# Performance work log

Hardware: AMD Instinct MI355X
Metric: run time of the kernel (lower is better)

## Reference

```python
import jax, jax.numpy as jnp
import numpy as np

B, T, F, M = 32, 256, 512, 4   # batch, pred_len (=d_model=state_size), feature_dim (=mamba seq), time-mark feats
N = F - M                      # number of variates in x_enc
T2 = 2 * T
EPS = 1e-5


def setup_inputs() -> dict:
    key = jax.random.key(0)
    it = iter(jax.random.split(key, 32))
    def nrm(*s):
        return jax.random.normal(next(it), s, jnp.float32) * 0.02
    inp = {
        "x_enc": jax.random.normal(next(it), (B, T, N), jnp.float32),
        "x_mark_enc": jax.random.normal(next(it), (B, T, M), jnp.float32),
        "x_dec": jnp.zeros((1, 1, 1), jnp.float32),
        "x_mark_dec": jnp.zeros((1, 1, 1), jnp.float32),
        # 3 structurally identical MambaBlocks -> stack params on leading dim 3
        "norm_w": jnp.ones((3, T), jnp.float32),
        "inp_W": nrm(3, T, T2), "inp_b": jnp.zeros((3, T2), jnp.float32),
        "conv_W": nrm(3, F, F, 3), "conv_b": jnp.zeros((3, F), jnp.float32),
        "convlin_W": nrm(3, T2, T2), "convlin_b": jnp.zeros((3, T2), jnp.float32),
        "fc1_W": nrm(3, T2, T2), "fc1_b": jnp.zeros((3, T2), jnp.float32),
        "fc2_W": nrm(3, T2, T), "fc2_b": jnp.zeros((3, T), jnp.float32),
        "fc3_W": nrm(3, T2, T), "fc3_b": jnp.zeros((3, T), jnp.float32),
        "D_W": nrm(3, T, T2), "D_b": jnp.zeros((3, T2), jnp.float32),
        "out_W": nrm(3, T2, T), "out_b": jnp.ones((3, T), jnp.float32),  # out_proj.bias init to 1.0
        "proj_W": nrm(T, T), "proj_b": jnp.zeros((T,), jnp.float32),
    }
    return inp


def _rmsnorm(x, w):
    return x * jax.lax.rsqrt(jnp.mean(x * x, -1, keepdims=True) + EPS) * w


def _conv1d(x, W, b):
    # x: [B, C, L], W: [C_out, C_in, 3], padding=1
    y = jax.lax.conv_general_dilated(x, W, (1,), [(1, 1)], dimension_numbers=("NCH", "OIH", "NCH"))
    return y + b[None, :, None]


def _s6(x, fc1W, fc1b, fc2W, fc2b, fc3W, fc3b):
    # h is zero-initialized each call, so dA=exp(delta*A) multiplies zeros and
    # y = einsum('bln,bldn->bld', C, x[...,None]*dB) = delta * x * <C,B>_n
    Bmat = x @ fc2W + fc2b                         # [B, L, n]
    Cmat = x @ fc3W + fc3b                         # [B, L, n]
    delta = jax.nn.softplus(x @ fc1W + fc1b)       # [B, L, d]
    cb = jnp.einsum("bln,bln->bl", Cmat, Bmat)   # contraction over state dim
    return delta * x * cb[:, :, None]


def _block(x, i, p):
    xn = _rmsnorm(x, p["norm_w"][i])
    xp = xn @ p["inp_W"][i] + p["inp_b"][i]                      # [B, F, 2T]
    xc = jax.nn.silu(_conv1d(xp, p["conv_W"][i], p["conv_b"][i]))
    xco = xc @ p["convlin_W"][i] + p["convlin_b"][i]
    xssm = _s6(xco, p["fc1_W"][i], p["fc1_b"][i], p["fc2_W"][i], p["fc2_b"][i], p["fc3_W"][i], p["fc3_b"][i])
    xres = jax.nn.silu(xn @ p["D_W"][i] + p["D_b"][i])
    return (jax.nn.silu(xssm) * xres) @ p["out_W"][i] + p["out_b"][i]


def _forward(x_enc, x_mark_enc, p):
    means = jax.lax.stop_gradient(jnp.mean(x_enc, 1, keepdims=True))  # detached in torch
    xe = x_enc - means
    stdev = jnp.sqrt(jnp.var(xe, axis=1, keepdims=True) + 1e-5)       # NOT detached in torch
    xe = xe / stdev
    x = jnp.concatenate([xe, x_mark_enc], axis=2).transpose(0, 2, 1)  # [B, F, T]
    for i in range(3):
        x = _block(x, i, p)
    dec = (x @ p["proj_W"] + p["proj_b"]).transpose(0, 2, 1)          # [B, T, F]
    return dec[:, :, :N] * stdev + means                              # pred_len == T


def reference(x_enc, x_mark_enc, x_dec, x_mark_dec, norm_w, inp_W, inp_b, conv_W, conv_b, convlin_W, convlin_b, fc1_W, fc1_b, fc2_W, fc2_b, fc3_W, fc3_b, D_W, D_b, out_W, out_b, proj_W, proj_b):
    p = dict(norm_w=norm_w, inp_W=inp_W, inp_b=inp_b, conv_W=conv_W, conv_b=conv_b, convlin_W=convlin_W, convlin_b=convlin_b, fc1_W=fc1_W, fc1_b=fc1_b, fc2_W=fc2_W, fc2_b=fc2_b, fc3_W=fc3_W, fc3_b=fc3_b, D_W=D_W, D_b=D_b, out_W=out_W, out_b=out_b, proj_W=proj_W, proj_b=proj_b)
    return _forward(x_enc, x_mark_enc, p)
```

## Files before the change

### kernel.cpp

```cpp
#include <hip/hip_runtime.h>
#include <hip/hip_bf16.h>
#include <math.h>

typedef __hip_bfloat16 bf16;
typedef short short8 __attribute__((ext_vector_type(8)));
typedef short short4v __attribute__((ext_vector_type(4)));
typedef float floatx4 __attribute__((ext_vector_type(4)));

constexpr int CB_ = 32;
constexpr int CT = 256;
constexpr int CF = 512;
constexpr int CN = 508;
constexpr int CM = 4;
constexpr int CT2 = 512;
constexpr int MROWS = CB_ * CF;
constexpr int PADL = 528;

__device__ __forceinline__ float b2f(bf16 v) { return __bfloat162float(v); }
__device__ __forceinline__ bf16 f2b(float v) { return __float2bfloat16(v); }
__device__ __forceinline__ float s2f(short s) {
    unsigned u = ((unsigned)(unsigned short)s) << 16;
    return __builtin_bit_cast(float, u);
}
__device__ __forceinline__ short f2s(float v) {
    bf16 t = __float2bfloat16(v);
    return __builtin_bit_cast(short, t);
}
__device__ __forceinline__ float silu_f(float x) { return x / (1.0f + __expf(-x)); }
__device__ __forceinline__ float softplus_f(float x) {
    return fmaxf(x, 0.0f) + __logf(1.0f + __expf(-fabsf(x)));
}

__device__ __forceinline__ void gl_lds16(const bf16* g, short* l) {
    __builtin_amdgcn_global_load_lds(
        (const __attribute__((address_space(1))) unsigned int*)(g),
        (__attribute__((address_space(3))) unsigned int*)(l), 16, 0, 0);
}

constexpr int CONVN = 3 * 3 * 512 * 512;
constexpr int MTILES = 3520;
struct P8 { const float* s[8]; bf16* d[8]; };
__global__ __launch_bounds__(256) void prepack_all_kernel(P8 p, const float* __restrict__ nw,
                                                          const float* __restrict__ convW,
                                                          bf16* __restrict__ convD,
                                                          bf16* __restrict__ xpT,
                                                          float* __restrict__ CBv) {
    int bid = blockIdx.x;
    if (bid >= MTILES) {
        int idx = (bid - MTILES) * 256 + threadIdx.x;
        if (idx < CONVN) {
            int ci = idx & 511;
            int co = (idx >> 9) & 511;
            int it = idx >> 18;
            int tap = it % 3, ib = it / 3;
            convD[idx] = f2b(convW[(((size_t)(ib * 512 + co)) * 512 + ci) * 3 + tap]);
        } else if (idx < CONVN + 32768) {
            int j = idx - CONVN;
            int ci = j & 511;
            int w = (j >> 9) & 1;
            int b = j >> 10;
            xpT[((size_t)b * PADL + (w ? 513 : 0)) * 512 + ci] = f2b(0.0f);
        } else if (idx < CONVN + 32768 + MROWS) {
            CBv[idx - CONVN - 32768] = 0.0f;
        }
        return;
    }
    const int Ks[8]   = {256, 256, 512, 512, 512, 512, 512, 256};
    const int Ns[8]   = {512, 512, 512, 256, 256, 512, 256, 256};
    const int zs[8]   = {3, 3, 3, 3, 3, 3, 3, 1};
    const int dstr[8] = {262144, 262144, 524288, 524288, 524288, 262144, 131072, 65536};
    const int rml[8]  = {1, 1, 1, 2, 2, 1, 1, 1};
    const int rad[8]  = {0, 0, 0, 0, 1, 0, 0, 0};
    int m = 0, acc = 0;
    for (m = 0; m < 8; m++) {
        int c = (Ns[m] >> 5) * (Ks[m] >> 5) * zs[m];
        if (bid < acc + c) break;
        acc += c;
    }
    int lid = bid - acc;
    int K = Ks[m], N = Ns[m];
    int tx = N >> 5, ty = K >> 5;
    int z = lid / (tx * ty), rem = lid % (tx * ty);
    int k0 = (rem / tx) * 32, n0 = (rem % tx) * 32;
    const float* s = p.s[m] + (size_t)z * K * N;
    bf16* d = p.d[m] + (size_t)z * dstr[m];
    int mul = rml[m], add = rad[m];
    bool fold = (m <= 1);
    __shared__ float Ts[32][33];
    for (int e = threadIdx.x; e < 1024; e += 256) {
        int r = e >> 5, c = e & 31;
        float v = s[(size_t)(k0 + r) * N + n0 + c];
        if (fold) v *= nw[z * 256 + k0 + r];
        Ts[r][c] = v;
    }
    __syncthreads();
    for (int e = threadIdx.x; e < 1024; e += 256) {
        int r = e >> 5, c = e & 31;
        d[(size_t)((n0 + r) * mul + add) * K + k0 + c] = f2b(Ts[c][r]);
    }
}

__global__ __launch_bounds__(256) void buildx_kernel(
    const float* __restrict__ xe, const float* __restrict__ xm,
    float* __restrict__ means, float* __restrict__ stdev,
    bf16* __restrict__ X0, float* __restrict__ SCL) {
    __shared__ float L[256][65];
    __shared__ float red_s[4][64], red_q[4][64];
    __shared__ float stat_m[64], stat_i[64];
    int blk = blockIdx.x;
    int b = blk >> 3, f0 = (blk & 7) * 64;
    int tid = threadIdx.x;
    int j = tid & 63, tq = tid >> 6;
    int f = f0 + j;
    float ps = 0.f, pq = 0.f;
    const float* xep = xe + (size_t)b * CT * CN + f;
    const float* xmp = xm + (size_t)b * CT * CM + (f - CN);
    #pragma unroll 4
    for (int tt = 0; tt < 64; tt++) {
        int t = tq * 64 + tt;
        float v = (f < CN) ? xep[(size_t)t * CN] : xmp[(size_t)t * CM];
        L[t][j] = v;
        ps += v;
        pq += v * v;
    }
    red_s[tq][j] = ps;
    red_q[tq][j] = pq;
    __syncthreads();
    if (tid < 64) {
        int ff = f0 + tid;
        float s = red_s[0][tid] + red_s[1][tid] + red_s[2][tid] + red_s[3][tid];
        float q = red_q[0][tid] + red_q[1][tid] + red_q[2][tid] + red_q[3][tid];
        float mean, isd, msq;
        if (ff < CN) {
            mean = s * (1.0f / 256.0f);
            float var = fmaxf(q * (1.0f / 256.0f) - mean * mean, 0.0f);
            float sd = sqrtf(var + 1e-5f);
            isd = 1.0f / sd;
            means[b * CN + ff] = mean;
            stdev[b * CN + ff] = sd;
            msq = var / (var + 1e-5f);
        } else {
            mean = 0.0f;
            isd = 1.0f;
            msq = q * (1.0f / 256.0f);
        }
        stat_m[tid] = mean;
        stat_i[tid] = isd;
        SCL[b * 512 + ff] = rsqrtf(msq + 1e-5f);
    }
    __syncthreads();
    bf16* outp = X0 + ((size_t)(b * 512 + f0)) * 256;
    int t = tid;
    #pragma unroll 4
    for (int fp = 0; fp < 64; fp++) {
        float val = (L[t][fp] - stat_m[fp]) * stat_i[fp];
        outp[(size_t)fp * 256 + t] = f2b(val);
    }
}

template <int MODE>
__global__ __launch_bounds__(256) void mgemm_kernel(const bf16* __restrict__ A,
                                                    const bf16* __restrict__ Wt,
                                                    const float* __restrict__ b1,
                                                    const float* __restrict__ b2,
                                                    const float* __restrict__ SCL,
                                                    bf16* __restrict__ o1,
                                                    bf16* __restrict__ o2,
                                                    int K, int Ncols) {
    __shared__ __align__(16) short As[128 * 32];
    __shared__ __align__(16) short Bs[128 * 32];
    const int tid = threadIdx.x;
    const int lane = tid & 63;
    const int wave = tid >> 6;
    const int m0 = blockIdx.x * 128, n0 = blockIdx.y * 128;

    const int srow0 = wave * 32;
    const int lrow = lane >> 2;
    const int lcol = (lane & 3) * 8;

    const bf16* aP0 = A + (size_t)(m0 + srow0 + lrow) * K + lcol;
    const bf16* aP1 = A + (size_t)(m0 + srow0 + 16 + lrow) * K + lcol;
    const bf16* bP0 = Wt + (size_t)(n0 + srow0 + lrow) * K + lcol;
    const bf16* bP1 = Wt + (size_t)(n0 + srow0 + 16 + lrow) * K + lcol;
    short* aL0 = &As[srow0 * 32];
    short* aL1 = &As[(srow0 + 16) * 32];
    short* bL0 = &Bs[srow0 * 32];
    short* bL1 = &Bs[(srow0 + 16) * 32];

    const int wm = (wave & 1) * 64, wn = (wave >> 1) * 64;
    const int fr = lane & 15, quad = lane >> 4;

    floatx4 acc[4][4];
    #pragma unroll
    for (int i = 0; i < 4; i++)
        #pragma unroll
        for (int j = 0; j < 4; j++) acc[i][j] = (floatx4){0.f, 0.f, 0.f, 0.f};

    for (int k0 = 0; k0 < K; k0 += 32) {
        gl_lds16(aP0 + k0, aL0);
        gl_lds16(aP1 + k0, aL1);
        gl_lds16(bP0 + k0, bL0);
        gl_lds16(bP1 + k0, bL1);
        __syncthreads();
        short8 af[4], bfv[4];
        #pragma unroll
        for (int i = 0; i < 4; i++) af[i] = *(const short8*)&As[(wm + i * 16 + fr) * 32 + quad * 8];
        #pragma unroll
        for (int j = 0; j < 4; j++) bfv[j] = *(const short8*)&Bs[(wn + j * 16 + fr) * 32 + quad * 8];
        #pragma unroll
        for (int i = 0; i < 4; i++)
            #pragma unroll
            for (int j = 0; j < 4; j++)
                acc[i][j] = __builtin_amdgcn_mfma_f32_16x16x32_bf16(af[i], bfv[j], acc[i][j], 0, 0, 0);
        __syncthreads();
    }

    if (MODE == 0) {
        #pragma unroll
        for (int j = 0; j < 4; j++) {
            int n = n0 + wn + j * 16 + fr;
            float bv = b1[n];
            #pragma unroll
            for (int i = 0; i < 4; i++) {
                int mb = m0 + wm + i * 16 + quad * 4;
                #pragma unroll
                for (int r = 0; r < 4; r++)
                    o1[(size_t)(mb + r) * Ncols + n] = f2b(acc[i][j][r] + bv);
            }
        }
    } else {
        if (n0 + wn < 512) {
            int b = (m0 + wm) >> 9;
            #pragma unroll
            for (int i = 0; i < 4; i++) {
                int mb = m0 + wm + i * 16 + quad * 4;
                float sclr[4];
                #pragma unroll
                for (int r = 0; r < 4; r++) sclr[r] = SCL[mb + r];
                #pragma unroll
                for (int j = 0; j < 4; j++) {
                    int n = n0 + wn + j * 16 + fr;
                    float bv = b1[n];
                    bf16* dst = o1 + ((size_t)b * PADL + n + 1) * 512;
                    int ci = mb & 511;
                    short4v pk;
                    #pragma unroll
                    for (int r = 0; r < 4; r++) pk[r] = f2s(acc[i][j][r] * sclr[r] + bv);
                    *(short4v*)(dst + ci) = pk;
                }
            }
        } else {
            #pragma unroll
            for (int i = 0; i < 4; i++) {
                int mb = m0 + wm + i * 16 + quad * 4;
                float sclr[4];
                #pragma unroll
                for (int r = 0; r < 4; r++) sclr[r] = SCL[mb + r];
                #pragma unroll
                for (int j = 0; j < 4; j++) {
                    int n = n0 + wn + j * 16 + fr;
                    float bv = b2[n - 512];
                    #pragma unroll
                    for (int r = 0; r < 4; r++)
                        o2[(size_t)(mb + r) * 512 + (n - 512)] =
                            f2b(silu_f(acc[i][j][r] * sclr[r] + bv));
                }
            }
        }
    }
}

__global__ __launch_bounds__(256) void cbgemm_kernel(const bf16* __restrict__ A,
                                                     const bf16* __restrict__ Wt,
                                                     const float* __restrict__ b2,
                                                     const float* __restrict__ b3,
                                                     float* __restrict__ CBv) {
    __shared__ __align__(16) short As[128 * 32];
    __shared__ __align__(16) short Bs[128 * 32];
    const int tid = threadIdx.x;
    const int lane = tid & 63;
    const int wave = tid >> 6;
    const int m0 = blockIdx.x * 128, n0 = blockIdx.y * 128;

    const int srow0 = wave * 32;
    const int lrow = lane >> 2;
    const int lcol = (lane & 3) * 8;
    const bf16* aP0 = A + (size_t)(m0 + srow0 + lrow) * 512 + lcol;
    const bf16* aP1 = A + (size_t)(m0 + srow0 + 16 + lrow) * 512 + lcol;
    const bf16* bP0 = Wt + (size_t)(n0 + srow0 + lrow) * 512 + lcol;
    const bf16* bP1 = Wt + (size_t)(n0 + srow0 + 16 + lrow) * 512 + lcol;
    short* aL0 = &As[srow0 * 32];
    short* aL1 = &As[(srow0 + 16) * 32];
    short* bL0 = &Bs[srow0 * 32];
    short* bL1 = &Bs[(srow0 + 16) * 32];

    const int wm = (wave & 1) * 64, wn = (wave >> 1) * 64;
    const int fr = lane & 15, quad = lane >> 4;

    floatx4 acc[4][4];
    #pragma unroll
    for (int i = 0; i < 4; i++)
        #pragma unroll
        for (int j = 0; j < 4; j++) acc[i][j] = (floatx4){0.f, 0.f, 0.f, 0.f};

    for (int k0 = 0; k0 < 512; k0 += 32) {
        gl_lds16(aP0 + k0, aL0);
        gl_lds16(aP1 + k0, aL1);
        gl_lds16(bP0 + k0, bL0);
        gl_lds16(bP1 + k0, bL1);
        __syncthreads();
        short8 af[4], bfv[4];
        #pragma unroll
        for (int i = 0; i < 4; i++) af[i] = *(const short8*)&As[(wm + i * 16 + fr) * 32 + quad * 8];
        #pragma unroll
        for (int j = 0; j < 4; j++) bfv[j] = *(const short8*)&Bs[(wn + j * 16 + fr) * 32 + quad * 8];
        #pragma unroll
        for (int i = 0; i < 4; i++)
            #pragma unroll
            for (int j = 0; j < 4; j++)
                acc[i][j] = __builtin_amdgcn_mfma_f32_16x16x32_bf16(af[i], bfv[j], acc[i][j], 0, 0, 0);
        __syncthreads();
    }
    int nnb = n0 + wn;
    float bv[4];
    #pragma unroll
    for (int j = 0; j < 4; j++) {
        int nn = nnb + j * 16 + fr;
        int c = nn >> 1;
        bv[j] = (fr & 1) ? b3[c] : b2[c];
    }
    #pragma unroll
    for (int i = 0; i < 4; i++) {
        #pragma unroll
        for (int r = 0; r < 4; r++) {
            float s = 0.f;
            #pragma unroll
            for (int j = 0; j < 4; j++) {
                float v = acc[i][j][r] + bv[j];
                s += v * __shfl_xor(v, 1);
            }
            s += __shfl_xor(s, 2);
            s += __shfl_xor(s, 4);
            s += __shfl_xor(s, 8);
            if (fr == 0)
                atomicAdd(&CBv[m0 + wm + i * 16 + quad * 4 + r], s * 0.5f);
        }
    }
}

__global__ __launch_bounds__(256) void fc1gate_kernel(const bf16* __restrict__ A,
                                                      const bf16* __restrict__ Wt,
                                                      const float* __restrict__ b1,
                                                      const float* __restrict__ CBv,
                                                      const bf16* __restrict__ Xres,
                                                      bf16* __restrict__ G) {
    __shared__ __align__(16) short As[128 * 32];
    __shared__ __align__(16) short Bs[128 * 32];
    const int tid = threadIdx.x;
    const int lane = tid & 63;
    const int wave = tid >> 6;
    const int m0 = blockIdx.x * 128, n0 = blockIdx.y * 128;

    const int srow0 = wave * 32;
    const int lrow = lane >> 2;
    const int lcol = (lane & 3) * 8;
    const bf16* aP0 = A + (size_t)(m0 + srow0 + lrow) * 512 + lcol;
    const bf16* aP1 = A + (size_t)(m0 + srow0 + 16 + lrow) * 512 + lcol;
    const bf16* bP0 = Wt + (size_t)(n0 + srow0 + lrow) * 512 + lcol;
    const bf16* bP1 = Wt + (size_t)(n0 + srow0 + 16 + lrow) * 512 + lcol;
    short* aL0 = &As[srow0 * 32];
    short* aL1 = &As[(srow0 + 16) * 32];
    short* bL0 = &Bs[srow0 * 32];
    short* bL1 = &Bs[(srow0 + 16) * 32];

    const int wm = (wave & 1) * 64, wn = (wave >> 1) * 64;
    const int fr = lane & 15, quad = lane >> 4;

    floatx4 acc[4][4];
    #pragma unroll
    for (int i = 0; i < 4; i++)
        #pragma unroll
        for (int j = 0; j < 4; j++) acc[i][j] = (floatx4){0.f, 0.f, 0.f, 0.f};

    for (int k0 = 0; k0 < 512; k0 += 32) {
        gl_lds16(aP0 + k0, aL0);
        gl_lds16(aP1 + k0, aL1);
        gl_lds16(bP0 + k0, bL0);
        gl_lds16(bP1 + k0, bL1);
        __syncthreads();
        short8 af[4], bfv[4];
        #pragma unroll
        for (int i = 0; i < 4; i++) af[i] = *(const short8*)&As[(wm + i * 16 + fr) * 32 + quad * 8];
        #pragma unroll
        for (int j = 0; j < 4; j++) bfv[j] = *(const short8*)&Bs[(wn + j * 16 + fr) * 32 + quad * 8];
        #pragma unroll
        for (int i = 0; i < 4; i++)
            #pragma unroll
            for (int j = 0; j < 4; j++)
                acc[i][j] = __builtin_amdgcn_mfma_f32_16x16x32_bf16(af[i], bfv[j], acc[i][j], 0, 0, 0);
        __syncthreads();
    }
    #pragma unroll
    for (int i = 0; i < 4; i++) {
        int mb = m0 + wm + i * 16 + quad * 4;
        float cbr[4];
        #pragma unroll
        for (int r = 0; r < 4; r++) cbr[r] = CBv[mb + r];
        #pragma unroll
        for (int j = 0; j < 4; j++) {
            int n = n0 + wn + j * 16 + fr;
            float bv = b1[n];
            #pragma unroll
            for (int r = 0; r < 4; r++) {
                size_t off = (size_t)(mb + r) * 512 + n;
                float delta = softplus_f(acc[i][j][r] + bv);
                float xssm = delta * b2f(A[off]) * cbr[r];
                G[off] = f2b(silu_f(xssm) * b2f(Xres[off]));
            }
        }
    }
}

__global__ __launch_bounds__(256) void conv_mfma_kernel(const bf16* __restrict__ Wc,
                                                        const bf16* __restrict__ xpT,
                                                        const float* __restrict__ bias,
                                                        bf16* __restrict__ Out,
                                                        float* __restrict__ CBvZ) {
    __shared__ __align__(16) short As[3 * 128 * 32];
    __shared__ __align__(16) short Bs[144 * 32];
    const int tid = threadIdx.x;
    const int lane = tid & 63;
    const int wave = tid >> 6;
    int bx = blockIdx.x;
    if (bx < 128 && tid < 128) CBvZ[bx * 128 + tid] = 0.0f;
    int xcd = bx & 7, g = bx >> 3;
    int mt = g & 3;
    int id = xcd * 16 + (g >> 2);
    int nt = id & 3, b = id >> 2;
    const int m0 = mt * 128, n0 = nt * 128;
    const bf16* xb = xpT + (size_t)b * PADL * 512;

    const int lrow = lane >> 2;
    const int lcol = (lane & 3) * 8;
    const int wm = (wave & 1) * 64, wn = (wave >> 1) * 64;
    const int fr = lane & 15, quad = lane >> 4;

    floatx4 acc[4][4];
    #pragma unroll
    for (int i = 0; i < 4; i++)
        #pragma unroll
        for (int j = 0; j < 4; j++) acc[i][j] = (floatx4){0.f, 0.f, 0.f, 0.f};

    for (int k0 = 0; k0 < 512; k0 += 32) {
        for (int ga = wave; ga < 24; ga += 4) {
            int tap = ga >> 3, rg = ga & 7;
            gl_lds16(Wc + (size_t)tap * 262144 + (size_t)(m0 + rg * 16 + lrow) * 512 + k0 + lcol,
                     &As[ga * 512]);
        }
        for (int gb = wave; gb < 9; gb += 4) {
            gl_lds16(xb + (size_t)(n0 + gb * 16 + lrow) * 512 + k0 + lcol, &Bs[gb * 512]);
        }
        __syncthreads();
        #pragma unroll
        for (int tap = 0; tap < 3; tap++) {
            short8 af[4], bfv[4];
            #pragma unroll
            for (int i = 0; i < 4; i++)
                af[i] = *(const short8*)&As[tap * 4096 + (wm + i * 16 + fr) * 32 + quad * 8];
            #pragma unroll
            for (int j = 0; j < 4; j++)
                bfv[j] = *(const short8*)&Bs[(wn + j * 16 + fr + tap) * 32 + quad * 8];
            #pragma unroll
            for (int i = 0; i < 4; i++)
                #pragma unroll
                for (int j = 0; j < 4; j++)
                    acc[i][j] = __builtin_amdgcn_mfma_f32_16x16x32_bf16(af[i], bfv[j], acc[i][j], 0, 0, 0);
        }
        __syncthreads();
    }
    bf16* ob = Out + (size_t)b * CF * CT2;
    #pragma unroll
    for (int i = 0; i < 4; i++) {
        int mb = m0 + wm + i * 16 + quad * 4;
        #pragma unroll
        for (int r = 0; r < 4; r++) {
            float bv = bias[mb + r];
            #pragma unroll
            for (int j = 0; j < 4; j++) {
                int n = n0 + wn + j * 16 + fr;
                ob[(size_t)(mb + r) * CT2 + n] = f2b(silu_f(acc[i][j][r] + bv));
            }
        }
    }
}

__global__ __launch_bounds__(256) void gemm_scl_kernel(const bf16* __restrict__ A,
                                                       const bf16* __restrict__ Wt,
                                                       const float* __restrict__ bias,
                                                       bf16* __restrict__ Xo,
                                                       float* __restrict__ SCL) {
    __shared__ __align__(16) short As[64 * 32];
    __shared__ __align__(16) short Bs[256 * 32];
    __shared__ float red[4][64];
    const int tid = threadIdx.x;
    const int lane = tid & 63;
    const int wave = tid >> 6;
    const int m0 = blockIdx.x * 64;

    const int lrow = lane >> 2;
    const int lcol = (lane & 3) * 8;
    const bf16* aP = A + (size_t)(m0 + wave * 16 + lrow) * 512 + lcol;
    short* aL = &As[wave * 16 * 32];
    const bf16* bP[4];
    short* bL[4];
    #pragma unroll
    for (int g = 0; g < 4; g++) {
        int r0 = (wave * 4 + g) * 16;
        bP[g] = Wt + (size_t)(r0 + lrow) * 512 + lcol;
        bL[g] = &Bs[r0 * 32];
    }
    const int wn = wave * 64;
    const int fr = lane & 15, quad = lane >> 4;

    floatx4 acc[4][4];
    #pragma unroll
    for (int i = 0; i < 4; i++)
        #pragma unroll
        for (int j = 0; j < 4; j++) acc[i][j] = (floatx4){0.f, 0.f, 0.f, 0.f};

    for (int k0 = 0; k0 < 512; k0 += 32) {
        gl_lds16(aP + k0, aL);
        #pragma unroll
        for (int g = 0; g < 4; g++) gl_lds16(bP[g] + k0, bL[g]);
        __syncthreads();
        short8 af[4], bfv[4];
        #pragma unroll
        for (int i = 0; i < 4; i++) af[i] = *(const short8*)&As[(i * 16 + fr) * 32 + quad * 8];
        #pragma unroll
        for (int j = 0; j < 4; j++) bfv[j] = *(const short8*)&Bs[(wn + j * 16 + fr) * 32 + quad * 8];
        #pragma unroll
        for (int i = 0; i < 4; i++)
            #pragma unroll
            for (int j = 0; j < 4; j++)
                acc[i][j] = __builtin_amdgcn_mfma_f32_16x16x32_bf16(af[i], bfv[j], acc[i][j], 0, 0, 0);
        __syncthreads();
    }
    #pragma unroll
    for (int j = 0; j < 4; j++) {
        float bv = bias[wn + j * 16 + fr];
        #pragma unroll
        for (int i = 0; i < 4; i++)
            #pragma unroll
            for (int r = 0; r < 4; r++) acc[i][j][r] += bv;
    }
    #pragma unroll
    for (int i = 0; i < 4; i++) {
        #pragma unroll
        for (int r = 0; r < 4; r++) {
            float s = 0.f;
            #pragma unroll
            for (int j = 0; j < 4; j++) s += acc[i][j][r] * acc[i][j][r];
            #pragma unroll
            for (int o = 8; o > 0; o >>= 1) s += __shfl_xor(s, o);
            if (fr == 0) red[wave][i * 16 + quad * 4 + r] = s;
        }
    }
    __syncthreads();
    if (tid < 64) {
        float tot = red[0][tid] + red[1][tid] + red[2][tid] + red[3][tid];
        SCL[m0 + tid] = rsqrtf(tot * (1.0f / CT) + 1e-5f);
    }
    #pragma unroll
    for (int j = 0; j < 4; j++) {
        int n = wn + j * 16 + fr;
        #pragma unroll
        for (int i = 0; i < 4; i++) {
            int rl = i * 16 + quad * 4;
            #pragma unroll
            for (int r = 0; r < 4; r++)
                Xo[(size_t)(m0 + rl + r) * CT + n] = f2b(acc[i][j][r]);
        }
    }
}

__global__ __launch_bounds__(256) void proj_out_kernel(const bf16* __restrict__ A,
                                                       const bf16* __restrict__ Wt,
                                                       const float* __restrict__ bias,
                                                       const float* __restrict__ means,
                                                       const float* __restrict__ stdev,
                                                       float* __restrict__ out) {
    __shared__ __align__(16) short As[128 * 32];
    __shared__ __align__(16) short Bs[128 * 32];
    const int tid = threadIdx.x;
    const int lane = tid & 63;
    const int wave = tid >> 6;
    const int m0 = blockIdx.x * 128, n0 = blockIdx.y * 128;

    const int srow0 = wave * 32;
    const int lrow = lane >> 2;
    const int lcol = (lane & 3) * 8;
    const bf16* aP0 = A + (size_t)(m0 + srow0 + lrow) * 256 + lcol;
    const bf16* aP1 = A + (size_t)(m0 + srow0 + 16 + lrow) * 256 + lcol;
    const bf16* bP0 = Wt + (size_t)(n0 + srow0 + lrow) * 256 + lcol;
    const bf16* bP1 = Wt + (size_t)(n0 + srow0 + 16 + lrow) * 256 + lcol;
    short* aL0 = &As[srow0 * 32];
    short* aL1 = &As[(srow0 + 16) * 32];
    short* bL0 = &Bs[srow0 * 32];
    short* bL1 = &Bs[(srow0 + 16) * 32];

    const int wm = (wave & 1) * 64, wn = (wave >> 1) * 64;
    const int fr = lane & 15, quad = lane >> 4;

    floatx4 acc[4][4];
    #pragma unroll
    for (int i = 0; i < 4; i++)
        #pragma unroll
        for (int j = 0; j < 4; j++) acc[i][j] = (floatx4){0.f, 0.f, 0.f, 0.f};

    for (int k0 = 0; k0 < 256; k0 += 32) {
        gl_lds16(aP0 + k0, aL0);
        gl_lds16(aP1 + k0, aL1);
        gl_lds16(bP0 + k0, bL0);
        gl_lds16(bP1 + k0, bL1);
        __syncthreads();
        short8 af[4], bfv[4];
        #pragma unroll
        for (int i = 0; i < 4; i++) af[i] = *(const short8*)&As[(wm + i * 16 + fr) * 32 + quad * 8];
        #pragma unroll
        for (int j = 0; j < 4; j++) bfv[j] = *(const short8*)&Bs[(wn + j * 16 + fr) * 32 + quad * 8];
        #pragma unroll
        for (int i = 0; i < 4; i++)
            #pragma unroll
            for (int j = 0; j < 4; j++)
                acc[i][j] = __builtin_amdgcn_mfma_f32_16x16x32_bf16(af[i], bfv[j], acc[i][j], 0, 0, 0);
        __syncthreads();
    }
    #pragma unroll
    for (int j = 0; j < 4; j++) {
        int t = n0 + wn + j * 16 + fr;
        float bv = bias[t];
        #pragma unroll
        for (int i = 0; i < 4; i++) {
            int mb = m0 + wm + i * 16 + quad * 4;
            int b = mb >> 9;
            int nv = mb & 511;
            if (nv < CN) {
                floatx4 o;
                #pragma unroll
                for (int r = 0; r < 4; r++) {
                    int sn = b * CN + nv + r;
                    o[r] = (acc[i][j][r] + bv) * stdev[sn] + means[sn];
                }
                *(floatx4*)(out + ((size_t)(b * CT + t)) * CN + nv) = o;
            }
        }
    }
}

extern "C" void kernel_launch(void* const* d_in, const int* in_sizes, int n_in,
                              void* d_out, int out_size, void* d_ws, size_t ws_size,
                              hipStream_t stream) {
    const float* x_enc  = (const float*)d_in[0];
    const float* x_mark = (const float*)d_in[1];
    const float* norm_w = (const float*)d_in[4];
    const float* inp_W  = (const float*)d_in[5];
    const float* inp_b  = (const float*)d_in[6];
    const float* conv_W = (const float*)d_in[7];
    const float* conv_b = (const float*)d_in[8];
    const float* convlin_W = (const float*)d_in[9];
    const float* convlin_b = (const float*)d_in[10];
    const float* fc1_W = (const float*)d_in[11];
    const float* fc1_b = (const float*)d_in[12];
    const float* fc2_W = (const float*)d_in[13];
    const float* fc2_b = (const float*)d_in[14];
    const float* fc3_W = (const float*)d_in[15];
    const float* fc3_b = (const float*)d_in[16];
    const float* D_W   = (const float*)d_in[17];
    const float* D_b   = (const float*)d_in[18];
    const float* out_W = (const float*)d_in[19];
    const float* out_b = (const float*)d_in[20];
    const float* proj_W = (const float*)d_in[21];
    const float* proj_b = (const float*)d_in[22];

    char* ws = (char*)d_ws;
    float* MEANS = (float*)(ws);
    float* STDEV = (float*)(ws + 65536);
    float* CBv   = (float*)(ws + 131072);
    float* SCL   = (float*)(ws + 196608);
    bf16* wt = (bf16*)(ws + 262144);
    bf16* wt_g1      = wt;
    bf16* wt_g3      = wt + 786432;
    bf16* wt_convlin = wt + 2359296;
    bf16* wt_out     = wt + 3145728;
    bf16* wt_proj    = wt + 3538944;
    bf16* wt_conv    = wt + 3604480;
    bf16* xpT = (bf16*)(ws + 12189696);
    const size_t POOLB = 16777216;
    bf16* pool[4] = {
        (bf16*)(ws + 29491200),
        (bf16*)(ws + 29491200 + POOLB),
        (bf16*)(ws + 29491200 + 2 * POOLB),
        (bf16*)(ws + 29491200 + 3 * POOLB),
    };
    float* out = (float*)d_out;

    P8 p;
    p.s[0] = inp_W;  p.d[0] = wt_g1;
    p.s[1] = D_W;    p.d[1] = wt_g1 + 131072;
    p.s[2] = fc1_W;  p.d[2] = wt_g3;
    p.s[3] = fc2_W;  p.d[3] = wt_g3 + 262144;
    p.s[4] = fc3_W;  p.d[4] = wt_g3 + 262144;
    p.s[5] = convlin_W; p.d[5] = wt_convlin;
    p.s[6] = out_W;  p.d[6] = wt_out;
    p.s[7] = proj_W; p.d[7] = wt_proj;
    int convBlocks = (CONVN + 32768 + MROWS + 255) / 256;
    prepack_all_kernel<<<MTILES + convBlocks, 256, 0, stream>>>(
        p, norm_w, conv_W, wt_conv, xpT, CBv);

    buildx_kernel<<<256, 256, 0, stream>>>(x_enc, x_mark, MEANS, STDEV, pool[0], SCL);

    int ia = 0, ico = 1, ires = 2, iout = 3;
    for (int i = 0; i < 3; i++) {
        bf16* A  = pool[ia];
        bf16* XCO = pool[ico];
        bf16* XRES = pool[ires];
        bf16* OUTP = pool[iout];

        mgemm_kernel<1><<<dim3(128, 8), 256, 0, stream>>>(
            A, wt_g1 + (size_t)i * 262144, inp_b + i * CT2, D_b + i * CT2, SCL,
            xpT, XRES, 256, 1024);
        conv_mfma_kernel<<<512, 256, 0, stream>>>(wt_conv + (size_t)i * 786432, xpT,
                                                  conv_b + i * CF, A, CBv);
        mgemm_kernel<0><<<dim3(128, 4), 256, 0, stream>>>(
            A, wt_convlin + (size_t)i * 262144, convlin_b + i * CT2, nullptr, nullptr,
            XCO, nullptr, 512, 512);
        cbgemm_kernel<<<dim3(128, 4), 256, 0, stream>>>(
            XCO, wt_g3 + (size_t)i * 524288 + 262144, fc2_b + i * CT, fc3_b + i * CT, CBv);
        fc1gate_kernel<<<dim3(128, 4), 256, 0, stream>>>(
            XCO, wt_g3 + (size_t)i * 524288, fc1_b + i * CT2, CBv, XRES, A);
        gemm_scl_kernel<<<256, 256, 0, stream>>>(
            A, wt_out + (size_t)i * 131072, out_b + i * CT, OUTP, SCL);

        int na = iout, nco = ia, nres = ico, nout = ires;
        ia = na; ico = nco; ires = nres; iout = nout;
    }

    proj_out_kernel<<<dim3(128, 2), 256, 0, stream>>>(
        pool[ia], wt_proj, proj_b, MEANS, STDEV, out);
}
```

Measured before the change: 558.7 us.

## Fold fc2/fc3 projections into convlin weights and merge B·C GEMM

Precomputes composite weights (convlin followed by fc2/fc3) with a new per-call GEMM, plus folded biases, so the B/C projections are computed straight from the conv output in the same GEMM that produces the convlin output. The separate cbgemm launch and its reread of the convlin output are removed, and the merged kernel runs twice as many column tiles with the CB reduction in its epilogue. In exchange, weight composition now runs on every call, and the composed weights are rounded to bf16, which changes numerics slightly.

```diff
diff --git a/kernel.cpp b/kernel.cpp
--- a/kernel.cpp
+++ b/kernel.cpp
@@ -44,7 +44,15 @@
                                                           const float* __restrict__ convW,
                                                           bf16* __restrict__ convD,
                                                           bf16* __restrict__ xpT,
-                                                          float* __restrict__ CBv) {
+                                                          float* __restrict__ CBv,
+                                                          const float* __restrict__ clW,
+                                                          bf16* __restrict__ clPlain,
+                                                          const float* __restrict__ clb,
+                                                          const float* __restrict__ pf2W,
+                                                          const float* __restrict__ pf2b,
+                                                          const float* __restrict__ pf3W,
+                                                          const float* __restrict__ pf3b,
+                                                          float* __restrict__ bcb) {
     int bid = blockIdx.x;
     if (bid >= MTILES) {
         int idx = (bid - MTILES) * 256 + threadIdx.x;
@@ -62,13 +70,24 @@
             xpT[((size_t)b * PADL + (w ? 513 : 0)) * 512 + ci] = f2b(0.0f);
         } else if (idx < CONVN + 32768 + MROWS) {
             CBv[idx - CONVN - 32768] = 0.0f;
+        } else if (idx < CONVN + 49152 + 786432) {
+            int j = idx - CONVN - 49152;
+            clPlain[j] = f2b(clW[j]);
+        } else if (idx < CONVN + 49152 + 786432 + 1536) {
+            int t = idx - CONVN - 49152 - 786432;
+            int z = t >> 9, r = t & 511, c = r & 255, half = r >> 8;
+            const float* fw = (half ? pf3W : pf2W) + (size_t)z * 131072;
+            const float* cbp = clb + z * 512;
+            float s = (half ? pf3b : pf2b)[z * 256 + c];
+            for (int k = 0; k < 512; k++) s += cbp[k] * fw[k * 256 + c];
+            bcb[z * 512 + 2 * c + half] = s;
         }
         return;
     }
     const int Ks[8]   = {256, 256, 512, 512, 512, 512, 512, 256};
     const int Ns[8]   = {512, 512, 512, 256, 256, 512, 256, 256};
     const int zs[8]   = {3, 3, 3, 3, 3, 3, 3, 1};
-    const int dstr[8] = {262144, 262144, 524288, 524288, 524288, 262144, 131072, 65536};
+    const int dstr[8] = {262144, 262144, 524288, 524288, 524288, 524288, 131072, 65536};
     const int rml[8]  = {1, 1, 1, 2, 2, 1, 1, 1};
     const int rad[8]  = {0, 0, 0, 0, 1, 0, 0, 0};
     int m = 0, acc = 0;
@@ -97,6 +116,72 @@
     for (int e = threadIdx.x; e < 1024; e += 256) {
         int r = e >> 5, c = e & 31;
         d[(size_t)((n0 + r) * mul + add) * K + k0 + c] = f2b(Ts[c][r]);
+    }
+}
+
+__global__ __launch_bounds__(256) void compw_kernel(const bf16* __restrict__ Asrc,
+                                                    const bf16* __restrict__ Psrc,
+                                                    bf16* __restrict__ Dst) {
+    __shared__ __align__(16) short As[128 * 32];
+    __shared__ __align__(16) short Bs[128 * 32];
+    const int tid = threadIdx.x;
+    const int lane = tid & 63;
+    const int wave = tid >> 6;
+    const int m0 = blockIdx.x * 128, n0 = blockIdx.y * 128;
+    const int z = blockIdx.z;
+    const bf16* A = Asrc + (size_t)z * 524288;
+    const bf16* Wt = Psrc + (size_t)z * 262144;
+    bf16* o = Dst + (size_t)z * 524288;
+
+    const int srow0 = wave * 32;
+    const int lrow = lane >> 2;
+    const int lcol = (lane & 3) * 8;
+    const bf16* aP0 = A + (size_t)(m0 + srow0 + lrow) * 512 + lcol;
+    const bf16* aP1 = A + (size_t)(m0 + srow0 + 16 + lrow) * 512 + lcol;
+    const bf16* bP0 = Wt + (size_t)(n0 + srow0 + lrow) * 512 + lcol;
+    const bf16* bP1 = Wt + (size_t)(n0 + srow0 + 16 + lrow) * 512 + lcol;
+    short* aL0 = &As[srow0 * 32];
+    short* aL1 = &As[(srow0 + 16) * 32];
+    short* bL0 = &Bs[srow0 * 32];
+    short* bL1 = &Bs[(srow0 + 16) * 32];
+
+    const int wm = (wave & 1) * 64, wn = (wave >> 1) * 64;
+    const int fr = lane & 15, quad = lane >> 4;
+
+    floatx4 acc[4][4];
+    #pragma unroll
+    for (int i = 0; i < 4; i++)
+        #pragma unroll
+        for (int j = 0; j < 4; j++) acc[i][j] = (floatx4){0.f, 0.f, 0.f, 0.f};
+
+    for (int k0 = 0; k0 < 512; k0 += 32) {
+        gl_lds16(aP0 + k0, aL0);
+        gl_lds16(aP1 + k0, aL1);
+        gl_lds16(bP0 + k0, bL0);
+        gl_lds16(bP1 + k0, bL1);
+        __syncthreads();
+        short8 af[4], bfv[4];
+        #pragma unroll
+        for (int i = 0; i < 4; i++) af[i] = *(const short8*)&As[(wm + i * 16 + fr) * 32 + quad * 8];
+        #pragma unroll
+        for (int j = 0; j < 4; j++) bfv[j] = *(const short8*)&Bs[(wn + j * 16 + fr) * 32 + quad * 8];
+        #pragma unroll
+        for (int i = 0; i < 4; i++)
+            #pragma unroll
+            for (int j = 0; j < 4; j++)
+                acc[i][j] = __builtin_amdgcn_mfma_f32_16x16x32_bf16(af[i], bfv[j], acc[i][j], 0, 0, 0);
+        __syncthreads();
+    }
+    #pragma unroll
+    for (int j = 0; j < 4; j++) {
+        int n = n0 + wn + j * 16 + fr;
+        #pragma unroll
+        for (int i = 0; i < 4; i++) {
+            int mb = m0 + wm + i * 16 + quad * 4;
+            #pragma unroll
+            for (int r = 0; r < 4; r++)
+                o[(size_t)(mb + r) * 512 + n] = f2b(acc[i][j][r]);
+        }
     }
 }
 
@@ -163,7 +248,7 @@
                                                     const bf16* __restrict__ Wt,
                                                     const float* __restrict__ b1,
                                                     const float* __restrict__ b2,
-                                                    const float* __restrict__ SCL,
+                                                    float* __restrict__ SCL,
                                                     bf16* __restrict__ o1,
                                                     bf16* __restrict__ o2,
                                                     int K, int Ncols) {
@@ -215,7 +300,7 @@
         __syncthreads();
     }
 
-    if (MODE == 0) {
+    if (MODE == 0 || (MODE == 2 && n0 + wn < 512)) {
         #pragma unroll
         for (int j = 0; j < 4; j++) {
             int n = n0 + wn + j * 16 + fr;
@@ -226,6 +311,28 @@
                 #pragma unroll
                 for (int r = 0; r < 4; r++)
                     o1[(size_t)(mb + r) * Ncols + n] = f2b(acc[i][j][r] + bv);
+            }
+        }
+    } else if (MODE == 2) {
+        int nnb = n0 + wn - 512;
+        float bv[4];
+        #pragma unroll
+        for (int j = 0; j < 4; j++) bv[j] = b2[nnb + j * 16 + fr];
+        #pragma unroll
+        for (int i = 0; i < 4; i++) {
+            #pragma unroll
+            for (int r = 0; r < 4; r++) {
+                float s = 0.f;
+                #pragma unroll
+                for (int j = 0; j < 4; j++) {
+                    float v = acc[i][j][r] + bv[j];
+                    s += v * __shfl_xor(v, 1);
+                }
+                s += __shfl_xor(s, 2);
+                s += __shfl_xor(s, 4);
+                s += __shfl_xor(s, 8);
+                if (fr == 0)
+                    atomicAdd(&SCL[m0 + wm + i * 16 + quad * 4 + r], s * 0.5f);
             }
         }
     } else {
@@ -266,84 +373,6 @@
                             f2b(silu_f(acc[i][j][r] * sclr[r] + bv));
                 }
             }
-        }
-    }
-}
-
-__global__ __launch_bounds__(256) void cbgemm_kernel(const bf16* __restrict__ A,
-                                                     const bf16* __restrict__ Wt,
-                                                     const float* __restrict__ b2,
-                                                     const float* __restrict__ b3,
-                                                     float* __restrict__ CBv) {
-    __shared__ __align__(16) short As[128 * 32];
-    __shared__ __align__(16) short Bs[128 * 32];
-    const int tid = threadIdx.x;
-    const int lane = tid & 63;
-    const int wave = tid >> 6;
-    const int m0 = blockIdx.x * 128, n0 = blockIdx.y * 128;
-
-    const int srow0 = wave * 32;
-    const int lrow = lane >> 2;
-    const int lcol = (lane & 3) * 8;
-    const bf16* aP0 = A + (size_t)(m0 + srow0 + lrow) * 512 + lcol;
-    const bf16* aP1 = A + (size_t)(m0 + srow0 + 16 + lrow) * 512 + lcol;
-    const bf16* bP0 = Wt + (size_t)(n0 + srow0 + lrow) * 512 + lcol;
-    const bf16* bP1 = Wt + (size_t)(n0 + srow0 + 16 + lrow) * 512 + lcol;
-    short* aL0 = &As[srow0 * 32];
-    short* aL1 = &As[(srow0 + 16) * 32];
-    short* bL0 = &Bs[srow0 * 32];
-    short* bL1 = &Bs[(srow0 + 16) * 32];
-
-    const int wm = (wave & 1) * 64, wn = (wave >> 1) * 64;
-    const int fr = lane & 15, quad = lane >> 4;
-
-    floatx4 acc[4][4];
-    #pragma unroll
-    for (int i = 0; i < 4; i++)
-        #pragma unroll
-        for (int j = 0; j < 4; j++) acc[i][j] = (floatx4){0.f, 0.f, 0.f, 0.f};
-
-    for (int k0 = 0; k0 < 512; k0 += 32) {
-        gl_lds16(aP0 + k0, aL0);
-        gl_lds16(aP1 + k0, aL1);
-        gl_lds16(bP0 + k0, bL0);
-        gl_lds16(bP1 + k0, bL1);
-        __syncthreads();
-        short8 af[4], bfv[4];
-        #pragma unroll
-        for (int i = 0; i < 4; i++) af[i] = *(const short8*)&As[(wm + i * 16 + fr) * 32 + quad * 8];
-        #pragma unroll
-        for (int j = 0; j < 4; j++) bfv[j] = *(const short8*)&Bs[(wn + j * 16 + fr) * 32 + quad * 8];
-        #pragma unroll
-        for (int i = 0; i < 4; i++)
-            #pragma unroll
-            for (int j = 0; j < 4; j++)
-                acc[i][j] = __builtin_amdgcn_mfma_f32_16x16x32_bf16(af[i], bfv[j], acc[i][j], 0, 0, 0);
-        __syncthreads();
-    }
-    int nnb = n0 + wn;
-    float bv[4];
-    #pragma unroll
-    for (int j = 0; j < 4; j++) {
-        int nn = nnb + j * 16 + fr;
-        int c = nn >> 1;
-        bv[j] = (fr & 1) ? b3[c] : b2[c];
-    }
-    #pragma unroll
-    for (int i = 0; i < 4; i++) {
-        #pragma unroll
-        for (int r = 0; r < 4; r++) {
-            float s = 0.f;
-            #pragma unroll
-            for (int j = 0; j < 4; j++) {
-                float v = acc[i][j][r] + bv[j];
-                s += v * __shfl_xor(v, 1);
-            }
-            s += __shfl_xor(s, 2);
-            s += __shfl_xor(s, 4);
-            s += __shfl_xor(s, 8);
-            if (fr == 0)
-                atomicAdd(&CBv[m0 + wm + i * 16 + quad * 4 + r], s * 0.5f);
         }
     }
 }
@@ -687,20 +716,22 @@
     float* STDEV = (float*)(ws + 65536);
     float* CBv   = (float*)(ws + 131072);
     float* SCL   = (float*)(ws + 196608);
-    bf16* wt = (bf16*)(ws + 262144);
-    bf16* wt_g1      = wt;
-    bf16* wt_g3      = wt + 786432;
-    bf16* wt_convlin = wt + 2359296;
-    bf16* wt_out     = wt + 3145728;
-    bf16* wt_proj    = wt + 3538944;
-    bf16* wt_conv    = wt + 3604480;
-    bf16* xpT = (bf16*)(ws + 12189696);
+    bf16* wb = (bf16*)(ws + 262144);
+    bf16* wt_g1      = wb;
+    bf16* wt_g3      = wb + 786432;
+    bf16* wt_merged  = wb + 2359296;
+    bf16* wt_out     = wb + 3932160;
+    bf16* wt_proj    = wb + 4325376;
+    bf16* wt_conv    = wb + 4390912;
+    bf16* cl_plain   = wb + 6750208;
+    float* bcb = (float*)(ws + 15335424);
+    bf16* xpT = (bf16*)(ws + 15728640);
     const size_t POOLB = 16777216;
     bf16* pool[4] = {
-        (bf16*)(ws + 29491200),
-        (bf16*)(ws + 29491200 + POOLB),
-        (bf16*)(ws + 29491200 + 2 * POOLB),
-        (bf16*)(ws + 29491200 + 3 * POOLB),
+        (bf16*)(ws + 33554432),
+        (bf16*)(ws + 33554432 + POOLB),
+        (bf16*)(ws + 33554432 + 2 * POOLB),
+        (bf16*)(ws + 33554432 + 3 * POOLB),
     };
     float* out = (float*)d_out;
 
@@ -710,12 +741,16 @@
     p.s[2] = fc1_W;  p.d[2] = wt_g3;
     p.s[3] = fc2_W;  p.d[3] = wt_g3 + 262144;
     p.s[4] = fc3_W;  p.d[4] = wt_g3 + 262144;
-    p.s[5] = convlin_W; p.d[5] = wt_convlin;
+    p.s[5] = convlin_W; p.d[5] = wt_merged;
     p.s[6] = out_W;  p.d[6] = wt_out;
     p.s[7] = proj_W; p.d[7] = wt_proj;
-    int convBlocks = (CONVN + 32768 + MROWS + 255) / 256;
+    int tailN = CONVN + 49152 + 786432 + 1536;
+    int convBlocks = (tailN + 255) / 256;
     prepack_all_kernel<<<MTILES + convBlocks, 256, 0, stream>>>(
-        p, norm_w, conv_W, wt_conv, xpT, CBv);
+        p, norm_w, conv_W, wt_conv, xpT, CBv,
+        convlin_W, cl_plain, convlin_b, fc2_W, fc2_b, fc3_W, fc3_b, bcb);
+
+    compw_kernel<<<dim3(4, 4, 3), 256, 0, stream>>>(wt_g3 + 262144, cl_plain, wt_merged + 262144);
 
     buildx_kernel<<<256, 256, 0, stream>>>(x_enc, x_mark, MEANS, STDEV, pool[0], SCL);
 
@@ -731,11 +766,9 @@
             xpT, XRES, 256, 1024);
         conv_mfma_kernel<<<512, 256, 0, stream>>>(wt_conv + (size_t)i * 786432, xpT,
                                                   conv_b + i * CF, A, CBv);
-        mgemm_kernel<0><<<dim3(128, 4), 256, 0, stream>>>(
-            A, wt_convlin + (size_t)i * 262144, convlin_b + i * CT2, nullptr, nullptr,
+        mgemm_kernel<2><<<dim3(128, 8), 256, 0, stream>>>(
+            A, wt_merged + (size_t)i * 524288, convlin_b + i * CT2, bcb + i * 512, CBv,
             XCO, nullptr, 512, 512);
-        cbgemm_kernel<<<dim3(128, 4), 256, 0, stream>>>(
-            XCO, wt_g3 + (size_t)i * 524288 + 262144, fc2_b + i * CT, fc3_b + i * CT, CBv);
         fc1gate_kernel<<<dim3(128, 4), 256, 0, stream>>>(
             XCO, wt_g3 + (size_t)i * 524288, fc1_b + i * CT2, CBv, XRES, A);
         gemm_scl_kernel<<<256, 256, 0, stream>>>(
```

New measurement: 588.9 us. 1.05x slower.
